# Kernel tuning notes

Hardware: AMD Instinct MI355X
Metric: run time of the kernel (lower is better)

The kernel has to match this reference:

```python
import jax, jax.numpy as jnp
import numpy as np

NODES = 14      # input_size: nodes per graph
IN_F = 24       # seq_len: node feature dim
HID1 = 32
HID2 = 64       # hid_feats
HEADS = 2
OUT = 24        # output_size
B = 2048        # number of graphs
SLOPE = 0.2


def _make_edges():
    # fully connected (no self loops) within each 14-node graph
    pairs = np.array([(i, j) for i in range(NODES) for j in range(NODES) if i != j]).T  # [2,182]
    offs = (np.arange(B) * NODES)[:, None]
    src = (pairs[0][None, :] + offs).reshape(-1)
    dst = (pairs[1][None, :] + offs).reshape(-1)
    return np.stack([src, dst]).astype(np.int32)  # [2, 372736]


def setup_inputs() -> dict:
    key = jax.random.key(0)
    ks = jax.random.split(key, 16)
    N = B * NODES
    x = jax.random.normal(ks[0], (N, IN_F), dtype=jnp.float32)
    y = jax.random.normal(ks[1], (N, OUT), dtype=jnp.float32)
    edge_index = jnp.asarray(_make_edges())
    batch = jnp.repeat(jnp.arange(B, dtype=jnp.int32), NODES)
    s = 0.1
    params = dict(
        W1=jax.random.normal(ks[2], (IN_F, HEADS * HID1), dtype=jnp.float32) * s,
        a_src1=jax.random.normal(ks[3], (HEADS, HID1), dtype=jnp.float32) * s,
        a_dst1=jax.random.normal(ks[4], (HEADS, HID1), dtype=jnp.float32) * s,
        b1=jnp.zeros((HID1,), dtype=jnp.float32),
        W2=jax.random.normal(ks[5], (HID1, HEADS * HID2), dtype=jnp.float32) * s,
        a_src2=jax.random.normal(ks[6], (HEADS, HID2), dtype=jnp.float32) * s,
        a_dst2=jax.random.normal(ks[7], (HEADS, HID2), dtype=jnp.float32) * s,
        b2=jnp.zeros((HID2,), dtype=jnp.float32),
        Wf1=jax.random.normal(ks[8], (NODES, HID2, 8), dtype=jnp.float32) * s,
        bf1=jnp.zeros((NODES, 8), dtype=jnp.float32),
        Wf2=jax.random.normal(ks[9], (NODES, 8, OUT), dtype=jnp.float32) * s,
        bf2=jnp.zeros((NODES, OUT), dtype=jnp.float32),
    )
    return {"x": x, "y": y, "edge_index": edge_index, "batch": batch, **params}


def gat_conv(x, src, dst, W, a_src, a_dst, b):
    # PyG GATConv, concat=False (mean over heads), self-loops already in src/dst
    N = x.shape[0]
    H, F = a_src.shape
    xh = (x @ W).reshape(N, H, F)                       # [N,H,F]
    al_s = (xh * a_src).sum(-1)                         # [N,H]
    al_d = (xh * a_dst).sum(-1)                         # [N,H]
    alpha = jax.nn.leaky_relu(al_s[src] + al_d[dst], SLOPE)  # [E,H]
    amax = jax.ops.segment_max(alpha, dst, num_segments=N)
    ex = jnp.exp(alpha - amax[dst])
    den = jax.ops.segment_sum(ex, dst, num_segments=N)
    w = ex / den[dst]                                   # softmax per target node
    out = jax.ops.segment_sum(w[:, :, None] * xh[src], dst, num_segments=N)  # [N,H,F]
    return out.mean(axis=1) + b


def reference(x, y, edge_index, batch, W1, a_src1, a_dst1, b1, W2, a_src2, a_dst2, b2, Wf1, bf1, Wf2, bf2):
    N = x.shape[0]
    loops = jnp.arange(N, dtype=edge_index.dtype)
    src = jnp.concatenate([edge_index[0], loops])
    dst = jnp.concatenate([edge_index[1], loops])
    h = jax.nn.elu(gat_conv(x, src, dst, W1, a_src1, a_dst1, b1))   # [N,32]
    h = gat_conv(h, src, dst, W2, a_src2, a_dst2, b2)               # [N,64]
    # batch regroup: batch ids are contiguous per graph, so the Python
    # gather-loop in the original is exactly a reshape
    nb = N // NODES
    xg = h.reshape(nb, NODES, HID2).transpose(1, 0, 2)   # [14, B, 64]
    yg = y.reshape(nb, NODES, OUT)                       # [B, 14, out]
    # per-node-index MLP ensemble, batched over the 14 indices
    hh = jax.nn.relu(jnp.einsum('kbh,kho->kbo', xg, Wf1) + bf1[:, None, :])
    pred = jax.nn.sigmoid(jnp.einsum('kbo,kop->kbp', hh, Wf2) + bf2[:, None, :])  # [14,B,out]
    return pred, yg
```

## Files before the change

### kernel.cpp

```cpp
#include <hip/hip_runtime.h>

#define NODES 14
#define IN_F 24
#define HID1 32
#define HID2 64
#define OUT_F 24
#define SLOPE 0.2f

#define XS_S 28
#define H1_S 36
#define H2_S 68

#define U_US1 0
#define U_UD1 48
#define U_US2 96
#define U_UD2 160

#define PHASE_FENCE() __builtin_amdgcn_sched_barrier(0)

__global__ __launch_bounds__(256) void compute_uvecs(
    const float* __restrict__ W1, const float* __restrict__ a_src1,
    const float* __restrict__ a_dst1,
    const float* __restrict__ W2, const float* __restrict__ a_src2,
    const float* __restrict__ a_dst2, float* __restrict__ u)
{
  const int tid = threadIdx.x;
  if (tid < 96) {
    const int sd = (tid >= 48), r = tid - sd * 48;
    const int h = (r >= IN_F), k = r - h * IN_F;
    const float* av = sd ? a_dst1 : a_src1;
    float s = 0.f;
#pragma unroll
    for (int f = 0; f < HID1; ++f)
      s += W1[k * 64 + h * HID1 + f] * av[h * HID1 + f];
    u[(sd ? U_UD1 : U_US1) + h * IN_F + k] = s;
  } else if (tid < 224) {
    const int j = tid - 96;
    const int sd = (j >= 64), r = j - sd * 64;
    const int h = (r >= HID1), k = r - h * HID1;
    const float* av = sd ? a_dst2 : a_src2;
    float s = 0.f;
#pragma unroll
    for (int f = 0; f < HID2; ++f)
      s += W2[k * 128 + h * HID2 + f] * av[h * HID2 + f];
    u[(sd ? U_UD2 : U_US2) + h * HID1 + k] = s;
  }
}

__global__ __launch_bounds__(128) void gnn_fused(
    const float* __restrict__ x, const float* __restrict__ y,
    const float* __restrict__ W1, const float* __restrict__ b1,
    const float* __restrict__ W2, const float* __restrict__ b2,
    const float* __restrict__ Wf1, const float* __restrict__ bf1,
    const float* __restrict__ Wf2, const float* __restrict__ bf2,
    const float* __restrict__ uvec,
    float* __restrict__ out, int ngraphs)
{
  const int g = blockIdx.x;
  const int tid = threadIdx.x;
  const int lane = tid & 63;
  const int wid = tid >> 6;

  __shared__ __align__(16) float xs[NODES * XS_S];
  __shared__ __align__(16) float h1s[NODES * H1_S];
  __shared__ __align__(16) float h2s[NODES * H2_S];
  __shared__ __align__(16) float wt[28 * 16];
  __shared__ float als[28], ald[28];
  __shared__ __align__(16) float hhs[112];

  float w1r[IN_F];
#pragma unroll
  for (int k = 0; k < IN_F; ++k) w1r[k] = W1[k * 64 + lane];

  float4 u1v[6];
  if (wid == 0 && lane < 56) {
    const int h = (lane >> 1) & 1, sd = lane & 1;
    const float* uu = uvec + (sd ? U_UD1 : U_US1) + h * IN_F;
#pragma unroll
    for (int k4 = 0; k4 < 6; ++k4) u1v[k4] = *(const float4*)&uu[k4 * 4];
  }

  if (tid < (NODES * OUT_F) / 4) {
    const float4* y4 = (const float4*)(y + (size_t)g * (NODES * OUT_F));
    float4* o4 = (float4*)(out + (size_t)NODES * ngraphs * OUT_F
                               + (size_t)g * (NODES * OUT_F));
    o4[tid] = y4[tid];
  }
  if (tid < (NODES * IN_F) / 4) {
    const float4 v = *(const float4*)(x + (size_t)g * (NODES * IN_F) + tid * 4);
    const int n = (tid * 4) / IN_F, k = (tid * 4) - n * IN_F;
    *(float4*)&xs[n * XS_S + k] = v;
  }
  __syncthreads();
  PHASE_FENCE();

  float xcol[NODES];
  {
#pragma unroll 2
    for (int n = 0; n < NODES; ++n) {
      float acc = 0.f;
#pragma unroll
      for (int k4 = 0; k4 < IN_F / 4; ++k4) {
        const float4 xv = *(const float4*)&xs[n * XS_S + k4 * 4];
        acc += xv.x * w1r[k4 * 4 + 0] + xv.y * w1r[k4 * 4 + 1]
             + xv.z * w1r[k4 * 4 + 2] + xv.w * w1r[k4 * 4 + 3];
      }
      xcol[n] = acc;
    }
  }
  PHASE_FENCE();
  if (wid == 0) {
    if (lane < 56) {
      const int n = lane >> 2, sd = lane & 1;
      float s = 0.f;
#pragma unroll
      for (int k4 = 0; k4 < 6; ++k4) {
        const float4 xv = *(const float4*)&xs[n * XS_S + k4 * 4];
        s += xv.x * u1v[k4].x + xv.y * u1v[k4].y
           + xv.z * u1v[k4].z + xv.w * u1v[k4].w;
      }
      (sd ? ald : als)[((lane >> 2) << 1) | ((lane >> 1) & 1)] = s;
      (void)n;
    }
    if (lane < NODES * 2) {
      const int h = lane & 1;
      const float ad = ald[lane];
      float a[NODES]; float m = -1e30f;
#pragma unroll
      for (int i = 0; i < NODES; ++i) {
        float v = als[i * 2 + h] + ad;
        v = v > 0.f ? v : SLOPE * v;
        a[i] = v; m = fmaxf(m, v);
      }
      float den = 0.f;
#pragma unroll
      for (int i = 0; i < NODES; ++i) { a[i] = __expf(a[i] - m); den += a[i]; }
      const float r = 1.f / den;
      float* wr = &wt[lane * 16];
      *(float4*)&wr[0]  = make_float4(a[0]*r,  a[1]*r,  a[2]*r,  a[3]*r);
      *(float4*)&wr[4]  = make_float4(a[4]*r,  a[5]*r,  a[6]*r,  a[7]*r);
      *(float4*)&wr[8]  = make_float4(a[8]*r,  a[9]*r,  a[10]*r, a[11]*r);
      *(float2*)&wr[12] = make_float2(a[12]*r, a[13]*r);
    }
  }
  float w2r[HID1];
#pragma unroll
  for (int k = 0; k < HID1; ++k) w2r[k] = W2[k * 128 + tid];
  __syncthreads();
  PHASE_FENCE();

  {
    const int h = lane >> 5, f5 = lane & 31;
    const float bb = b1[f5];
#pragma unroll 2
    for (int tt = 0; tt < NODES / 2; ++tt) {
      const int n = wid * (NODES / 2) + tt;
      const float* wr = &wt[(n * 2 + h) * 16];
      const float4 w0 = *(const float4*)&wr[0];
      const float4 w1 = *(const float4*)&wr[4];
      const float4 w2 = *(const float4*)&wr[8];
      const float2 w3 = *(const float2*)&wr[12];
      float o = w0.x*xcol[0] + w0.y*xcol[1] + w0.z*xcol[2] + w0.w*xcol[3]
              + w1.x*xcol[4] + w1.y*xcol[5] + w1.z*xcol[6] + w1.w*xcol[7]
              + w2.x*xcol[8] + w2.y*xcol[9] + w2.z*xcol[10] + w2.w*xcol[11]
              + w3.x*xcol[12] + w3.y*xcol[13];
      const float oo = __shfl_xor(o, 32);
      if (h == 0) {
        const float v = 0.5f * (o + oo) + bb;
        h1s[n * H1_S + f5] = v > 0.f ? v : expm1f(v);
      }
    }
  }
  __syncthreads();
  PHASE_FENCE();

  float x2c[NODES];
  {
#pragma unroll 2
    for (int n = 0; n < NODES; ++n) {
      float acc = 0.f;
#pragma unroll
      for (int k4 = 0; k4 < HID1 / 4; ++k4) {
        const float4 hv = *(const float4*)&h1s[n * H1_S + k4 * 4];
        acc += hv.x * w2r[k4 * 4 + 0] + hv.y * w2r[k4 * 4 + 1]
             + hv.z * w2r[k4 * 4 + 2] + hv.w * w2r[k4 * 4 + 3];
      }
      x2c[n] = acc;
    }
  }
  PHASE_FENCE();
  if (wid == 0) {
    if (lane < 56) {
      const int n = lane >> 2, h = (lane >> 1) & 1, sd = lane & 1;
      const float* uu = uvec + (sd ? U_UD2 : U_US2) + h * HID1;
      float s = 0.f;
#pragma unroll
      for (int k4 = 0; k4 < 8; ++k4) {
        const float4 hv = *(const float4*)&h1s[n * H1_S + k4 * 4];
        const float4 uv = *(const float4*)&uu[k4 * 4];
        s += hv.x * uv.x + hv.y * uv.y + hv.z * uv.z + hv.w * uv.w;
      }
      (sd ? ald : als)[n * 2 + h] = s;
    }
    if (lane < NODES * 2) {
      const int h = lane & 1;
      const float ad = ald[lane];
      float a[NODES]; float m = -1e30f;
#pragma unroll
      for (int i = 0; i < NODES; ++i) {
        float v = als[i * 2 + h] + ad;
        v = v > 0.f ? v : SLOPE * v;
        a[i] = v; m = fmaxf(m, v);
      }
      float den = 0.f;
#pragma unroll
      for (int i = 0; i < NODES; ++i) { a[i] = __expf(a[i] - m); den += a[i]; }
      const float r = 1.f / den;
      float* wr = &wt[lane * 16];
      *(float4*)&wr[0]  = make_float4(a[0]*r,  a[1]*r,  a[2]*r,  a[3]*r);
      *(float4*)&wr[4]  = make_float4(a[4]*r,  a[5]*r,  a[6]*r,  a[7]*r);
      *(float4*)&wr[8]  = make_float4(a[8]*r,  a[9]*r,  a[10]*r, a[11]*r);
      *(float2*)&wr[12] = make_float2(a[12]*r, a[13]*r);
    }
  }
  float wf[32];
  if (tid < NODES * 8) {
    const int k = tid >> 3, e = tid & 7;
#pragma unroll
    for (int f = 0; f < 32; ++f) wf[f] = Wf1[(k * HID2 + f) * 8 + e];
  }
  __syncthreads();
  PHASE_FENCE();

  {
    float agg[NODES];
#pragma unroll
    for (int n = 0; n < NODES; ++n) {
      const float* wr = &wt[(n * 2 + wid) * 16];
      const float4 w0 = *(const float4*)&wr[0];
      const float4 w1 = *(const float4*)&wr[4];
      const float4 w2 = *(const float4*)&wr[8];
      const float2 w3 = *(const float2*)&wr[12];
      agg[n] = w0.x*x2c[0] + w0.y*x2c[1] + w0.z*x2c[2] + w0.w*x2c[3]
             + w1.x*x2c[4] + w1.y*x2c[5] + w1.z*x2c[6] + w1.w*x2c[7]
             + w2.x*x2c[8] + w2.y*x2c[9] + w2.z*x2c[10] + w2.w*x2c[11]
             + w3.x*x2c[12] + w3.y*x2c[13];
    }
    if (wid == 1) {
#pragma unroll
      for (int n = 0; n < NODES; ++n) h2s[n * H2_S + lane] = agg[n];
    }
    __syncthreads();
    if (wid == 0) {
      const float bb = b2[lane];
#pragma unroll
      for (int n = 0; n < NODES; ++n)
        h2s[n * H2_S + lane] = 0.5f * (agg[n] + h2s[n * H2_S + lane]) + bb;
    }
  }
  __syncthreads();
  PHASE_FENCE();

  if (tid < NODES * 8) {
    const int k = tid >> 3, e = tid & 7;
    float acc = bf1[k * 8 + e];
#pragma unroll
    for (int f4 = 0; f4 < 8; ++f4) {
      const float4 hv = *(const float4*)&h2s[k * H2_S + f4 * 4];
      acc += hv.x * wf[f4 * 4 + 0] + hv.y * wf[f4 * 4 + 1]
           + hv.z * wf[f4 * 4 + 2] + hv.w * wf[f4 * 4 + 3];
    }
#pragma unroll
    for (int f4 = 8; f4 < 16; ++f4) {
      const float4 hv = *(const float4*)&h2s[k * H2_S + f4 * 4];
      acc += hv.x * Wf1[(k * HID2 + f4 * 4 + 0) * 8 + e]
           + hv.y * Wf1[(k * HID2 + f4 * 4 + 1) * 8 + e]
           + hv.z * Wf1[(k * HID2 + f4 * 4 + 2) * 8 + e]
           + hv.w * Wf1[(k * HID2 + f4 * 4 + 3) * 8 + e];
    }
    hhs[tid] = fmaxf(acc, 0.f);
  }
  __syncthreads();
  PHASE_FENCE();

  for (int idx = tid; idx < NODES * OUT_F; idx += 128) {
    const int k = idx / OUT_F, o = idx - k * OUT_F;
    const float4 h0 = *(const float4*)&hhs[k * 8];
    const float4 h1 = *(const float4*)&hhs[k * 8 + 4];
    float acc = bf2[k * OUT_F + o]
              + h0.x * Wf2[(k * 8 + 0) * OUT_F + o]
              + h0.y * Wf2[(k * 8 + 1) * OUT_F + o]
              + h0.z * Wf2[(k * 8 + 2) * OUT_F + o]
              + h0.w * Wf2[(k * 8 + 3) * OUT_F + o]
              + h1.x * Wf2[(k * 8 + 4) * OUT_F + o]
              + h1.y * Wf2[(k * 8 + 5) * OUT_F + o]
              + h1.z * Wf2[(k * 8 + 6) * OUT_F + o]
              + h1.w * Wf2[(k * 8 + 7) * OUT_F + o];
    out[(size_t)k * ngraphs * OUT_F + (size_t)g * OUT_F + o] =
        1.f / (1.f + __expf(-acc));
  }
}

extern "C" void kernel_launch(void* const* d_in, const int* in_sizes, int n_in,
                              void* d_out, int out_size, void* d_ws, size_t ws_size,
                              hipStream_t stream) {
  const float* x      = (const float*)d_in[0];
  const float* y      = (const float*)d_in[1];
  const float* W1     = (const float*)d_in[4];
  const float* a_src1 = (const float*)d_in[5];
  const float* a_dst1 = (const float*)d_in[6];
  const float* b1     = (const float*)d_in[7];
  const float* W2     = (const float*)d_in[8];
  const float* a_src2 = (const float*)d_in[9];
  const float* a_dst2 = (const float*)d_in[10];
  const float* b2     = (const float*)d_in[11];
  const float* Wf1    = (const float*)d_in[12];
  const float* bf1    = (const float*)d_in[13];
  const float* Wf2    = (const float*)d_in[14];
  const float* bf2    = (const float*)d_in[15];
  float* out = (float*)d_out;
  float* u   = (float*)d_ws;

  const int nnodes  = in_sizes[0] / IN_F;
  const int ngraphs = nnodes / NODES;

  hipLaunchKernelGGL(compute_uvecs, dim3(1), dim3(256), 0, stream,
                     W1, a_src1, a_dst1, W2, a_src2, a_dst2, u);
  hipLaunchKernelGGL(gnn_fused, dim3(ngraphs), dim3(128), 0, stream,
                     x, y, W1, b1, W2, b2, Wf1, bf1, Wf2, bf2, u, out, ngraphs);
}
```

Measured before the change: 29.83 us.

## Split layer-2 work across waves and read x directly from global memory

After: 31.02 us. 1.04x slower.

```diff
diff --git a/kernel.cpp b/kernel.cpp
--- a/kernel.cpp
+++ b/kernel.cpp
@@ -7,7 +7,6 @@
 #define OUT_F 24
 #define SLOPE 0.2f
 
-#define XS_S 28
 #define H1_S 36
 #define H2_S 68
 
@@ -61,24 +60,13 @@
   const int lane = tid & 63;
   const int wid = tid >> 6;
 
-  __shared__ __align__(16) float xs[NODES * XS_S];
   __shared__ __align__(16) float h1s[NODES * H1_S];
   __shared__ __align__(16) float h2s[NODES * H2_S];
   __shared__ __align__(16) float wt[28 * 16];
-  __shared__ float als[28], ald[28];
+  __shared__ __align__(16) float als[32], ald[32];
   __shared__ __align__(16) float hhs[112];
 
-  float w1r[IN_F];
-#pragma unroll
-  for (int k = 0; k < IN_F; ++k) w1r[k] = W1[k * 64 + lane];
-
-  float4 u1v[6];
-  if (wid == 0 && lane < 56) {
-    const int h = (lane >> 1) & 1, sd = lane & 1;
-    const float* uu = uvec + (sd ? U_UD1 : U_US1) + h * IN_F;
-#pragma unroll
-    for (int k4 = 0; k4 < 6; ++k4) u1v[k4] = *(const float4*)&uu[k4 * 4];
-  }
+  const float* xg = x + (size_t)g * (NODES * IN_F);
 
   if (tid < (NODES * OUT_F) / 4) {
     const float4* y4 = (const float4*)(y + (size_t)g * (NODES * OUT_F));
@@ -86,49 +74,45 @@
                                + (size_t)g * (NODES * OUT_F));
     o4[tid] = y4[tid];
   }
-  if (tid < (NODES * IN_F) / 4) {
-    const float4 v = *(const float4*)(x + (size_t)g * (NODES * IN_F) + tid * 4);
-    const int n = (tid * 4) / IN_F, k = (tid * 4) - n * IN_F;
-    *(float4*)&xs[n * XS_S + k] = v;
-  }
-  __syncthreads();
-  PHASE_FENCE();
-
+
+  float w1r[IN_F];
+#pragma unroll
+  for (int k = 0; k < IN_F; ++k) w1r[k] = W1[k * 64 + lane];
   float xcol[NODES];
-  {
 #pragma unroll 2
-    for (int n = 0; n < NODES; ++n) {
-      float acc = 0.f;
-#pragma unroll
-      for (int k4 = 0; k4 < IN_F / 4; ++k4) {
-        const float4 xv = *(const float4*)&xs[n * XS_S + k4 * 4];
-        acc += xv.x * w1r[k4 * 4 + 0] + xv.y * w1r[k4 * 4 + 1]
-             + xv.z * w1r[k4 * 4 + 2] + xv.w * w1r[k4 * 4 + 3];
-      }
-      xcol[n] = acc;
-    }
-  }
-  PHASE_FENCE();
-  if (wid == 0) {
+  for (int n = 0; n < NODES; ++n) {
+    float acc = 0.f;
+#pragma unroll
+    for (int k = 0; k < IN_F; ++k) acc += xg[n * IN_F + k] * w1r[k];
+    xcol[n] = acc;
+  }
+  PHASE_FENCE();
+  if (wid == 1) {
     if (lane < 56) {
-      const int n = lane >> 2, sd = lane & 1;
+      const int n = lane >> 2, h = (lane >> 1) & 1, sd = lane & 1;
+      const float* uu = uvec + (sd ? U_UD1 : U_US1) + h * IN_F;
       float s = 0.f;
 #pragma unroll
       for (int k4 = 0; k4 < 6; ++k4) {
-        const float4 xv = *(const float4*)&xs[n * XS_S + k4 * 4];
-        s += xv.x * u1v[k4].x + xv.y * u1v[k4].y
-           + xv.z * u1v[k4].z + xv.w * u1v[k4].w;
-      }
-      (sd ? ald : als)[((lane >> 2) << 1) | ((lane >> 1) & 1)] = s;
-      (void)n;
+        const float4 xv = *(const float4*)&xg[n * IN_F + k4 * 4];
+        const float4 uv = *(const float4*)&uu[k4 * 4];
+        s += xv.x * uv.x + xv.y * uv.y + xv.z * uv.z + xv.w * uv.w;
+      }
+      (sd ? ald : als)[h * 16 + n] = s;
     }
     if (lane < NODES * 2) {
-      const int h = lane & 1;
-      const float ad = ald[lane];
-      float a[NODES]; float m = -1e30f;
+      const int j = lane >> 1, h = lane & 1;
+      const float ad = ald[h * 16 + j];
+      const float4 A0 = *(const float4*)&als[h * 16 + 0];
+      const float4 A1 = *(const float4*)&als[h * 16 + 4];
+      const float4 A2 = *(const float4*)&als[h * 16 + 8];
+      const float2 A3 = *(const float2*)&als[h * 16 + 12];
+      float a[NODES] = {A0.x, A0.y, A0.z, A0.w, A1.x, A1.y, A1.z, A1.w,
+                        A2.x, A2.y, A2.z, A2.w, A3.x, A3.y};
+      float m = -1e30f;
 #pragma unroll
       for (int i = 0; i < NODES; ++i) {
-        float v = als[i * 2 + h] + ad;
+        float v = a[i] + ad;
         v = v > 0.f ? v : SLOPE * v;
         a[i] = v; m = fmaxf(m, v);
       }
@@ -143,9 +127,6 @@
       *(float2*)&wr[12] = make_float2(a[12]*r, a[13]*r);
     }
   }
-  float w2r[HID1];
-#pragma unroll
-  for (int k = 0; k < HID1; ++k) w2r[k] = W2[k * 128 + tid];
   __syncthreads();
   PHASE_FENCE();
 
@@ -174,22 +155,36 @@
   __syncthreads();
   PHASE_FENCE();
 
-  float x2c[NODES];
-  {
+  float acc0[NODES], acc1[NODES];
+  if (wid == 0) {
+#pragma unroll
+    for (int n = 0; n < NODES; ++n) { acc0[n] = 0.f; acc1[n] = 0.f; }
+#pragma unroll
+    for (int c = 0; c < 2; ++c) {
+      float w2a[16], w2b[16];
+#pragma unroll
+      for (int j = 0; j < 16; ++j) {
+        w2a[j] = W2[(c * 16 + j) * 128 + lane];
+        w2b[j] = W2[(c * 16 + j) * 128 + 64 + lane];
+      }
 #pragma unroll 2
-    for (int n = 0; n < NODES; ++n) {
-      float acc = 0.f;
-#pragma unroll
-      for (int k4 = 0; k4 < HID1 / 4; ++k4) {
-        const float4 hv = *(const float4*)&h1s[n * H1_S + k4 * 4];
-        acc += hv.x * w2r[k4 * 4 + 0] + hv.y * w2r[k4 * 4 + 1]
-             + hv.z * w2r[k4 * 4 + 2] + hv.w * w2r[k4 * 4 + 3];
-      }
-      x2c[n] = acc;
-    }
-  }
-  PHASE_FENCE();
-  if (wid == 0) {
+      for (int n = 0; n < NODES; ++n) {
+        const float4 v0 = *(const float4*)&h1s[n * H1_S + c * 16 + 0];
+        const float4 v1 = *(const float4*)&h1s[n * H1_S + c * 16 + 4];
+        const float4 v2 = *(const float4*)&h1s[n * H1_S + c * 16 + 8];
+        const float4 v3 = *(const float4*)&h1s[n * H1_S + c * 16 + 12];
+        acc0[n] += v0.x*w2a[0] + v0.y*w2a[1] + v0.z*w2a[2] + v0.w*w2a[3]
+                 + v1.x*w2a[4] + v1.y*w2a[5] + v1.z*w2a[6] + v1.w*w2a[7]
+                 + v2.x*w2a[8] + v2.y*w2a[9] + v2.z*w2a[10] + v2.w*w2a[11]
+                 + v3.x*w2a[12] + v3.y*w2a[13] + v3.z*w2a[14] + v3.w*w2a[15];
+        acc1[n] += v0.x*w2b[0] + v0.y*w2b[1] + v0.z*w2b[2] + v0.w*w2b[3]
+                 + v1.x*w2b[4] + v1.y*w2b[5] + v1.z*w2b[6] + v1.w*w2b[7]
+                 + v2.x*w2b[8] + v2.y*w2b[9] + v2.z*w2b[10] + v2.w*w2b[11]
+                 + v3.x*w2b[12] + v3.y*w2b[13] + v3.z*w2b[14] + v3.w*w2b[15];
+      }
+      PHASE_FENCE();
+    }
+  } else {
     if (lane < 56) {
       const int n = lane >> 2, h = (lane >> 1) & 1, sd = lane & 1;
       const float* uu = uvec + (sd ? U_UD2 : U_US2) + h * HID1;
@@ -200,15 +195,21 @@
         const float4 uv = *(const float4*)&uu[k4 * 4];
         s += hv.x * uv.x + hv.y * uv.y + hv.z * uv.z + hv.w * uv.w;
       }
-      (sd ? ald : als)[n * 2 + h] = s;
+      (sd ? ald : als)[h * 16 + n] = s;
     }
     if (lane < NODES * 2) {
-      const int h = lane & 1;
-      const float ad = ald[lane];
-      float a[NODES]; float m = -1e30f;
+      const int j = lane >> 1, h = lane & 1;
+      const float ad = ald[h * 16 + j];
+      const float4 A0 = *(const float4*)&als[h * 16 + 0];
+      const float4 A1 = *(const float4*)&als[h * 16 + 4];
+      const float4 A2 = *(const float4*)&als[h * 16 + 8];
+      const float2 A3 = *(const float2*)&als[h * 16 + 12];
+      float a[NODES] = {A0.x, A0.y, A0.z, A0.w, A1.x, A1.y, A1.z, A1.w,
+                        A2.x, A2.y, A2.z, A2.w, A3.x, A3.y};
+      float m = -1e30f;
 #pragma unroll
       for (int i = 0; i < NODES; ++i) {
-        float v = als[i * 2 + h] + ad;
+        float v = a[i] + ad;
         v = v > 0.f ? v : SLOPE * v;
         a[i] = v; m = fmaxf(m, v);
       }
@@ -223,39 +224,32 @@
       *(float2*)&wr[12] = make_float2(a[12]*r, a[13]*r);
     }
   }
-  float wf[32];
-  if (tid < NODES * 8) {
-    const int k = tid >> 3, e = tid & 7;
-#pragma unroll
-    for (int f = 0; f < 32; ++f) wf[f] = Wf1[(k * HID2 + f) * 8 + e];
-  }
-  __syncthreads();
-  PHASE_FENCE();
-
-  {
-    float agg[NODES];
-#pragma unroll
+  __syncthreads();
+  PHASE_FENCE();
+
+  if (wid == 0) {
+    const float bb = b2[lane];
+#pragma unroll 2
     for (int n = 0; n < NODES; ++n) {
-      const float* wr = &wt[(n * 2 + wid) * 16];
-      const float4 w0 = *(const float4*)&wr[0];
-      const float4 w1 = *(const float4*)&wr[4];
-      const float4 w2 = *(const float4*)&wr[8];
-      const float2 w3 = *(const float2*)&wr[12];
-      agg[n] = w0.x*x2c[0] + w0.y*x2c[1] + w0.z*x2c[2] + w0.w*x2c[3]
-             + w1.x*x2c[4] + w1.y*x2c[5] + w1.z*x2c[6] + w1.w*x2c[7]
-             + w2.x*x2c[8] + w2.y*x2c[9] + w2.z*x2c[10] + w2.w*x2c[11]
-             + w3.x*x2c[12] + w3.y*x2c[13];
-    }
-    if (wid == 1) {
-#pragma unroll
-      for (int n = 0; n < NODES; ++n) h2s[n * H2_S + lane] = agg[n];
-    }
-    __syncthreads();
-    if (wid == 0) {
-      const float bb = b2[lane];
-#pragma unroll
-      for (int n = 0; n < NODES; ++n)
-        h2s[n * H2_S + lane] = 0.5f * (agg[n] + h2s[n * H2_S + lane]) + bb;
+      const float* wr0 = &wt[(n * 2 + 0) * 16];
+      const float* wr1 = &wt[(n * 2 + 1) * 16];
+      const float4 p0 = *(const float4*)&wr0[0];
+      const float4 p1 = *(const float4*)&wr0[4];
+      const float4 p2 = *(const float4*)&wr0[8];
+      const float2 p3 = *(const float2*)&wr0[12];
+      const float4 q0 = *(const float4*)&wr1[0];
+      const float4 q1 = *(const float4*)&wr1[4];
+      const float4 q2 = *(const float4*)&wr1[8];
+      const float2 q3 = *(const float2*)&wr1[12];
+      const float o0 = p0.x*acc0[0] + p0.y*acc0[1] + p0.z*acc0[2] + p0.w*acc0[3]
+                     + p1.x*acc0[4] + p1.y*acc0[5] + p1.z*acc0[6] + p1.w*acc0[7]
+                     + p2.x*acc0[8] + p2.y*acc0[9] + p2.z*acc0[10] + p2.w*acc0[11]
+                     + p3.x*acc0[12] + p3.y*acc0[13];
+      const float o1 = q0.x*acc1[0] + q0.y*acc1[1] + q0.z*acc1[2] + q0.w*acc1[3]
+                     + q1.x*acc1[4] + q1.y*acc1[5] + q1.z*acc1[6] + q1.w*acc1[7]
+                     + q2.x*acc1[8] + q2.y*acc1[9] + q2.z*acc1[10] + q2.w*acc1[11]
+                     + q3.x*acc1[12] + q3.y*acc1[13];
+      h2s[n * H2_S + lane] = 0.5f * (o0 + o1) + bb;
     }
   }
   __syncthreads();
@@ -265,13 +259,7 @@
     const int k = tid >> 3, e = tid & 7;
     float acc = bf1[k * 8 + e];
 #pragma unroll
-    for (int f4 = 0; f4 < 8; ++f4) {
-      const float4 hv = *(const float4*)&h2s[k * H2_S + f4 * 4];
-      acc += hv.x * wf[f4 * 4 + 0] + hv.y * wf[f4 * 4 + 1]
-           + hv.z * wf[f4 * 4 + 2] + hv.w * wf[f4 * 4 + 3];
-    }
-#pragma unroll
-    for (int f4 = 8; f4 < 16; ++f4) {
+    for (int f4 = 0; f4 < 16; ++f4) {
       const float4 hv = *(const float4*)&h2s[k * H2_S + f4 * 4];
       acc += hv.x * Wf1[(k * HID2 + f4 * 4 + 0) * 8 + e]
            + hv.y * Wf1[(k * HID2 + f4 * 4 + 1) * 8 + e]
```

## Assign one attention head per wave and drop cross-wave barriers

Applied to the files above, without the earlier changes.

Result: slower. 32.20 us (+8.0%).

```diff
diff --git a/kernel.cpp b/kernel.cpp
--- a/kernel.cpp
+++ b/kernel.cpp
@@ -7,7 +7,6 @@
 #define OUT_F 24
 #define SLOPE 0.2f
 
-#define XS_S 28
 #define H1_S 36
 #define H2_S 68
 
@@ -59,26 +58,19 @@
   const int g = blockIdx.x;
   const int tid = threadIdx.x;
   const int lane = tid & 63;
-  const int wid = tid >> 6;
-
-  __shared__ __align__(16) float xs[NODES * XS_S];
+  const int w = tid >> 6;
+  const int l5 = lane & 31;
+  const int kh = lane >> 5;
+
+  __shared__ __align__(16) float h1p[2][NODES * H1_S];
   __shared__ __align__(16) float h1s[NODES * H1_S];
-  __shared__ __align__(16) float h2s[NODES * H2_S];
-  __shared__ __align__(16) float wt[28 * 16];
-  __shared__ float als[28], ald[28];
+  __shared__ __align__(16) float wt1[2][NODES * 16];
+  __shared__ __align__(16) float wt2[2][NODES * 16];
+  __shared__ __align__(16) float als2[2][16], ald2[2][16];
+  __shared__ __align__(16) float h2p[2][NODES * H2_S];
   __shared__ __align__(16) float hhs[112];
 
-  float w1r[IN_F];
-#pragma unroll
-  for (int k = 0; k < IN_F; ++k) w1r[k] = W1[k * 64 + lane];
-
-  float4 u1v[6];
-  if (wid == 0 && lane < 56) {
-    const int h = (lane >> 1) & 1, sd = lane & 1;
-    const float* uu = uvec + (sd ? U_UD1 : U_US1) + h * IN_F;
-#pragma unroll
-    for (int k4 = 0; k4 < 6; ++k4) u1v[k4] = *(const float4*)&uu[k4 * 4];
-  }
+  const float* xg = x + (size_t)g * (NODES * IN_F);
 
   if (tid < (NODES * OUT_F) / 4) {
     const float4* y4 = (const float4*)(y + (size_t)g * (NODES * OUT_F));
@@ -86,96 +78,107 @@
                                + (size_t)g * (NODES * OUT_F));
     o4[tid] = y4[tid];
   }
-  if (tid < (NODES * IN_F) / 4) {
-    const float4 v = *(const float4*)(x + (size_t)g * (NODES * IN_F) + tid * 4);
-    const int n = (tid * 4) / IN_F, k = (tid * 4) - n * IN_F;
-    *(float4*)&xs[n * XS_S + k] = v;
-  }
-  __syncthreads();
-  PHASE_FENCE();
 
   float xcol[NODES];
   {
+    const int col = 32 * w + l5;
+    float w1r[12];
+#pragma unroll
+    for (int k = 0; k < 12; ++k) w1r[k] = W1[(kh * 12 + k) * 64 + col];
 #pragma unroll 2
     for (int n = 0; n < NODES; ++n) {
       float acc = 0.f;
 #pragma unroll
-      for (int k4 = 0; k4 < IN_F / 4; ++k4) {
-        const float4 xv = *(const float4*)&xs[n * XS_S + k4 * 4];
+      for (int k4 = 0; k4 < 3; ++k4) {
+        const float4 xv = *(const float4*)&xg[n * IN_F + kh * 12 + k4 * 4];
         acc += xv.x * w1r[k4 * 4 + 0] + xv.y * w1r[k4 * 4 + 1]
              + xv.z * w1r[k4 * 4 + 2] + xv.w * w1r[k4 * 4 + 3];
       }
       xcol[n] = acc;
     }
-  }
-  PHASE_FENCE();
-  if (wid == 0) {
-    if (lane < 56) {
-      const int n = lane >> 2, sd = lane & 1;
-      float s = 0.f;
-#pragma unroll
-      for (int k4 = 0; k4 < 6; ++k4) {
-        const float4 xv = *(const float4*)&xs[n * XS_S + k4 * 4];
-        s += xv.x * u1v[k4].x + xv.y * u1v[k4].y
-           + xv.z * u1v[k4].z + xv.w * u1v[k4].w;
-      }
-      (sd ? ald : als)[((lane >> 2) << 1) | ((lane >> 1) & 1)] = s;
-      (void)n;
-    }
-    if (lane < NODES * 2) {
-      const int h = lane & 1;
-      const float ad = ald[lane];
-      float a[NODES]; float m = -1e30f;
-#pragma unroll
-      for (int i = 0; i < NODES; ++i) {
-        float v = als[i * 2 + h] + ad;
-        v = v > 0.f ? v : SLOPE * v;
-        a[i] = v; m = fmaxf(m, v);
-      }
-      float den = 0.f;
-#pragma unroll
-      for (int i = 0; i < NODES; ++i) { a[i] = __expf(a[i] - m); den += a[i]; }
-      const float r = 1.f / den;
-      float* wr = &wt[lane * 16];
-      *(float4*)&wr[0]  = make_float4(a[0]*r,  a[1]*r,  a[2]*r,  a[3]*r);
-      *(float4*)&wr[4]  = make_float4(a[4]*r,  a[5]*r,  a[6]*r,  a[7]*r);
-      *(float4*)&wr[8]  = make_float4(a[8]*r,  a[9]*r,  a[10]*r, a[11]*r);
-      *(float2*)&wr[12] = make_float2(a[12]*r, a[13]*r);
-    }
-  }
-  float w2r[HID1];
-#pragma unroll
-  for (int k = 0; k < HID1; ++k) w2r[k] = W2[k * 128 + tid];
-  __syncthreads();
-  PHASE_FENCE();
-
+#pragma unroll
+    for (int n = 0; n < NODES; ++n) xcol[n] += __shfl_xor(xcol[n], 32);
+  }
+  PHASE_FENCE();
+
+  if (lane < 28) {
+    const int n = lane >> 1, sd = lane & 1;
+    const float* uu = uvec + (sd ? U_UD1 : U_US1) + w * IN_F;
+    float s = 0.f;
+#pragma unroll
+    for (int k4 = 0; k4 < 6; ++k4) {
+      const float4 xv = *(const float4*)&xg[n * IN_F + k4 * 4];
+      const float4 uv = *(const float4*)&uu[k4 * 4];
+      s += xv.x * uv.x + xv.y * uv.y + xv.z * uv.z + xv.w * uv.w;
+    }
+    (sd ? ald2 : als2)[w][n] = s;
+  }
+  if (lane < NODES) {
+    const float ad = ald2[w][lane];
+    const float4 A0 = *(const float4*)&als2[w][0];
+    const float4 A1 = *(const float4*)&als2[w][4];
+    const float4 A2 = *(const float4*)&als2[w][8];
+    const float2 A3 = *(const float2*)&als2[w][12];
+    float a[NODES] = {A0.x, A0.y, A0.z, A0.w, A1.x, A1.y, A1.z, A1.w,
+                      A2.x, A2.y, A2.z, A2.w, A3.x, A3.y};
+    float m = -1e30f;
+#pragma unroll
+    for (int i = 0; i < NODES; ++i) {
+      float v = a[i] + ad;
+      v = v > 0.f ? v : SLOPE * v;
+      a[i] = v; m = fmaxf(m, v);
+    }
+    float den = 0.f;
+#pragma unroll
+    for (int i = 0; i < NODES; ++i) { a[i] = __expf(a[i] - m); den += a[i]; }
+    const float r = 1.f / den;
+    float* wr = &wt1[w][lane * 16];
+    *(float4*)&wr[0]  = make_float4(a[0]*r,  a[1]*r,  a[2]*r,  a[3]*r);
+    *(float4*)&wr[4]  = make_float4(a[4]*r,  a[5]*r,  a[6]*r,  a[7]*r);
+    *(float4*)&wr[8]  = make_float4(a[8]*r,  a[9]*r,  a[10]*r, a[11]*r);
+    *(float2*)&wr[12] = make_float2(a[12]*r, a[13]*r);
+  }
   {
-    const int h = lane >> 5, f5 = lane & 31;
-    const float bb = b1[f5];
-#pragma unroll 2
-    for (int tt = 0; tt < NODES / 2; ++tt) {
-      const int n = wid * (NODES / 2) + tt;
-      const float* wr = &wt[(n * 2 + h) * 16];
+    const float bb = b1[l5];
+#pragma unroll
+    for (int t = 0; t < NODES / 2; ++t) {
+      const int n = kh * (NODES / 2) + t;
+      const float* wr = &wt1[w][n * 16];
       const float4 w0 = *(const float4*)&wr[0];
       const float4 w1 = *(const float4*)&wr[4];
       const float4 w2 = *(const float4*)&wr[8];
       const float2 w3 = *(const float2*)&wr[12];
-      float o = w0.x*xcol[0] + w0.y*xcol[1] + w0.z*xcol[2] + w0.w*xcol[3]
-              + w1.x*xcol[4] + w1.y*xcol[5] + w1.z*xcol[6] + w1.w*xcol[7]
-              + w2.x*xcol[8] + w2.y*xcol[9] + w2.z*xcol[10] + w2.w*xcol[11]
-              + w3.x*xcol[12] + w3.y*xcol[13];
-      const float oo = __shfl_xor(o, 32);
-      if (h == 0) {
-        const float v = 0.5f * (o + oo) + bb;
-        h1s[n * H1_S + f5] = v > 0.f ? v : expm1f(v);
-      }
-    }
+      const float o = w0.x*xcol[0] + w0.y*xcol[1] + w0.z*xcol[2] + w0.w*xcol[3]
+                    + w1.x*xcol[4] + w1.y*xcol[5] + w1.z*xcol[6] + w1.w*xcol[7]
+                    + w2.x*xcol[8] + w2.y*xcol[9] + w2.z*xcol[10] + w2.w*xcol[11]
+                    + w3.x*xcol[12] + w3.y*xcol[13];
+      h1p[w][n * H1_S + l5] = o + bb;
+    }
+  }
+  __syncthreads();
+  PHASE_FENCE();
+
+  if (lane < 56) {
+    const int n = 7 * w + (lane >> 3), f4 = (lane & 7) * 4;
+    const float4 A = *(const float4*)&h1p[0][n * H1_S + f4];
+    const float4 B = *(const float4*)&h1p[1][n * H1_S + f4];
+    float4 v;
+    v.x = 0.5f * (A.x + B.x); v.y = 0.5f * (A.y + B.y);
+    v.z = 0.5f * (A.z + B.z); v.w = 0.5f * (A.w + B.w);
+    v.x = v.x > 0.f ? v.x : expm1f(v.x);
+    v.y = v.y > 0.f ? v.y : expm1f(v.y);
+    v.z = v.z > 0.f ? v.z : expm1f(v.z);
+    v.w = v.w > 0.f ? v.w : expm1f(v.w);
+    *(float4*)&h1s[n * H1_S + f4] = v;
   }
   __syncthreads();
   PHASE_FENCE();
 
   float x2c[NODES];
   {
+    float w2r[HID1];
+#pragma unroll
+    for (int k = 0; k < HID1; ++k) w2r[k] = W2[k * 128 + 64 * w + lane];
 #pragma unroll 2
     for (int n = 0; n < NODES; ++n) {
       float acc = 0.f;
@@ -189,73 +192,58 @@
     }
   }
   PHASE_FENCE();
-  if (wid == 0) {
-    if (lane < 56) {
-      const int n = lane >> 2, h = (lane >> 1) & 1, sd = lane & 1;
-      const float* uu = uvec + (sd ? U_UD2 : U_US2) + h * HID1;
-      float s = 0.f;
-#pragma unroll
-      for (int k4 = 0; k4 < 8; ++k4) {
-        const float4 hv = *(const float4*)&h1s[n * H1_S + k4 * 4];
-        const float4 uv = *(const float4*)&uu[k4 * 4];
-        s += hv.x * uv.x + hv.y * uv.y + hv.z * uv.z + hv.w * uv.w;
-      }
-      (sd ? ald : als)[n * 2 + h] = s;
-    }
-    if (lane < NODES * 2) {
-      const int h = lane & 1;
-      const float ad = ald[lane];
-      float a[NODES]; float m = -1e30f;
-#pragma unroll
-      for (int i = 0; i < NODES; ++i) {
-        float v = als[i * 2 + h] + ad;
-        v = v > 0.f ? v : SLOPE * v;
-        a[i] = v; m = fmaxf(m, v);
-      }
-      float den = 0.f;
-#pragma unroll
-      for (int i = 0; i < NODES; ++i) { a[i] = __expf(a[i] - m); den += a[i]; }
-      const float r = 1.f / den;
-      float* wr = &wt[lane * 16];
-      *(float4*)&wr[0]  = make_float4(a[0]*r,  a[1]*r,  a[2]*r,  a[3]*r);
-      *(float4*)&wr[4]  = make_float4(a[4]*r,  a[5]*r,  a[6]*r,  a[7]*r);
-      *(float4*)&wr[8]  = make_float4(a[8]*r,  a[9]*r,  a[10]*r, a[11]*r);
-      *(float2*)&wr[12] = make_float2(a[12]*r, a[13]*r);
-    }
-  }
-  float wf[32];
-  if (tid < NODES * 8) {
-    const int k = tid >> 3, e = tid & 7;
-#pragma unroll
-    for (int f = 0; f < 32; ++f) wf[f] = Wf1[(k * HID2 + f) * 8 + e];
-  }
-  __syncthreads();
-  PHASE_FENCE();
-
+
+  if (lane < 28) {
+    const int n = lane >> 1, sd = lane & 1;
+    const float* uu = uvec + (sd ? U_UD2 : U_US2) + w * HID1;
+    float s = 0.f;
+#pragma unroll
+    for (int k4 = 0; k4 < 8; ++k4) {
+      const float4 hv = *(const float4*)&h1s[n * H1_S + k4 * 4];
+      const float4 uv = *(const float4*)&uu[k4 * 4];
+      s += hv.x * uv.x + hv.y * uv.y + hv.z * uv.z + hv.w * uv.w;
+    }
+    (sd ? ald2 : als2)[w][n] = s;
+  }
+  if (lane < NODES) {
+    const float ad = ald2[w][lane];
+    const float4 A0 = *(const float4*)&als2[w][0];
+    const float4 A1 = *(const float4*)&als2[w][4];
+    const float4 A2 = *(const float4*)&als2[w][8];
+    const float2 A3 = *(const float2*)&als2[w][12];
+    float a[NODES] = {A0.x, A0.y, A0.z, A0.w, A1.x, A1.y, A1.z, A1.w,
+                      A2.x, A2.y, A2.z, A2.w, A3.x, A3.y};
+    float m = -1e30f;
+#pragma unroll
+    for (int i = 0; i < NODES; ++i) {
+      float v = a[i] + ad;
+      v = v > 0.f ? v : SLOPE * v;
+      a[i] = v; m = fmaxf(m, v);
+    }
+    float den = 0.f;
+#pragma unroll
+    for (int i = 0; i < NODES; ++i) { a[i] = __expf(a[i] - m); den += a[i]; }
+    const float r = 1.f / den;
+    float* wr = &wt2[w][lane * 16];
+    *(float4*)&wr[0]  = make_float4(a[0]*r,  a[1]*r,  a[2]*r,  a[3]*r);
+    *(float4*)&wr[4]  = make_float4(a[4]*r,  a[5]*r,  a[6]*r,  a[7]*r);
+    *(float4*)&wr[8]  = make_float4(a[8]*r,  a[9]*r,  a[10]*r, a[11]*r);
+    *(float2*)&wr[12] = make_float2(a[12]*r, a[13]*r);
+  }
   {
-    float agg[NODES];
-#pragma unroll
+    const float bb = b2[lane];
+#pragma unroll 2
     for (int n = 0; n < NODES; ++n) {
-      const float* wr = &wt[(n * 2 + wid) * 16];
+      const float* wr = &wt2[w][n * 16];
       const float4 w0 = *(const float4*)&wr[0];
       const float4 w1 = *(const float4*)&wr[4];
       const float4 w2 = *(const float4*)&wr[8];
       const float2 w3 = *(const float2*)&wr[12];
-      agg[n] = w0.x*x2c[0] + w0.y*x2c[1] + w0.z*x2c[2] + w0.w*x2c[3]
-             + w1.x*x2c[4] + w1.y*x2c[5] + w1.z*x2c[6] + w1.w*x2c[7]
-             + w2.x*x2c[8] + w2.y*x2c[9] + w2.z*x2c[10] + w2.w*x2c[11]
-             + w3.x*x2c[12] + w3.y*x2c[13];
-    }
-    if (wid == 1) {
-#pragma unroll
-      for (int n = 0; n < NODES; ++n) h2s[n * H2_S + lane] = agg[n];
-    }
-    __syncthreads();
-    if (wid == 0) {
-      const float bb = b2[lane];
-#pragma unroll
-      for (int n = 0; n < NODES; ++n)
-        h2s[n * H2_S + lane] = 0.5f * (agg[n] + h2s[n * H2_S + lane]) + bb;
+      const float o = w0.x*x2c[0] + w0.y*x2c[1] + w0.z*x2c[2] + w0.w*x2c[3]
+                    + w1.x*x2c[4] + w1.y*x2c[5] + w1.z*x2c[6] + w1.w*x2c[7]
+                    + w2.x*x2c[8] + w2.y*x2c[9] + w2.z*x2c[10] + w2.w*x2c[11]
+                    + w3.x*x2c[12] + w3.y*x2c[13];
+      h2p[w][n * H2_S + lane] = o + bb;
     }
   }
   __syncthreads();
@@ -265,18 +253,13 @@
     const int k = tid >> 3, e = tid & 7;
     float acc = bf1[k * 8 + e];
 #pragma unroll
-    for (int f4 = 0; f4 < 8; ++f4) {
-      const float4 hv = *(const float4*)&h2s[k * H2_S + f4 * 4];
-      acc += hv.x * wf[f4 * 4 + 0] + hv.y * wf[f4 * 4 + 1]
-           + hv.z * wf[f4 * 4 + 2] + hv.w * wf[f4 * 4 + 3];
-    }
-#pragma unroll
-    for (int f4 = 8; f4 < 16; ++f4) {
-      const float4 hv = *(const float4*)&h2s[k * H2_S + f4 * 4];
-      acc += hv.x * Wf1[(k * HID2 + f4 * 4 + 0) * 8 + e]
-           + hv.y * Wf1[(k * HID2 + f4 * 4 + 1) * 8 + e]
-           + hv.z * Wf1[(k * HID2 + f4 * 4 + 2) * 8 + e]
-           + hv.w * Wf1[(k * HID2 + f4 * 4 + 3) * 8 + e];
+    for (int f4 = 0; f4 < 16; ++f4) {
+      const float4 A = *(const float4*)&h2p[0][k * H2_S + f4 * 4];
+      const float4 B = *(const float4*)&h2p[1][k * H2_S + f4 * 4];
+      acc += (0.5f * (A.x + B.x)) * Wf1[(k * HID2 + f4 * 4 + 0) * 8 + e]
+           + (0.5f * (A.y + B.y)) * Wf1[(k * HID2 + f4 * 4 + 1) * 8 + e]
+           + (0.5f * (A.z + B.z)) * Wf1[(k * HID2 + f4 * 4 + 2) * 8 + e]
+           + (0.5f * (A.w + B.w)) * Wf1[(k * HID2 + f4 * 4 + 3) * 8 + e];
     }
     hhs[tid] = fmaxf(acc, 0.f);
   }
```
